# Optimization experiments

Hardware: AMD Instinct MI355X
Metric: run time of the kernel (lower is better)

Reference implementation:

```python
import jax, jax.numpy as jnp
import numpy as np

B, T, C = 4, 2048, 1024


def wkv(k, v, w, u, reverse):
    """RWKV WKV scan with running-max stabilization.
    k, v: [B, T, C]; w, u: [C]. Returns y: [B, T, C]."""
    def step(carry, kv):
        num, den, mx = carry          # each [B, C]
        k_t, v_t = kv                 # each [B, C]
        ku = k_t + u
        m = jnp.maximum(mx, ku)
        e1 = jnp.exp(mx - m)
        e2 = jnp.exp(ku - m)
        y = (e1 * num + e2 * v_t) / (e1 * den + e2)
        # state update with decay w
        mw = mx + w
        mn = jnp.maximum(mw, k_t)
        e1s = jnp.exp(mw - mn)
        e2s = jnp.exp(k_t - mn)
        return (e1s * num + e2s * v_t, e1s * den + e2s, mn), y

    z = jnp.zeros_like(k[:, 0])
    init = (z, z, jnp.full_like(z, -1e38))
    ks = jnp.swapaxes(k, 0, 1)  # [T, B, C]
    vs = jnp.swapaxes(v, 0, 1)
    _, ys = jax.lax.scan(step, init, (ks, vs), reverse=reverse)
    return jnp.swapaxes(ys, 0, 1)


def setup_inputs() -> dict:
    key = jax.random.key(0)
    k1, k2, k3, k4, k5, k6, k7 = jax.random.split(key, 7)
    x = jax.random.normal(k1, (B, T, C), dtype=jnp.float32)
    rkv_w = jax.random.normal(k2, (6 * C, C), dtype=jnp.float32) / np.sqrt(C)
    out_w = jax.random.normal(k3, (C, 2 * C), dtype=jnp.float32) / np.sqrt(2 * C)
    time_decay = jax.random.uniform(k4, (C,), jnp.float32, -6.0, -5.0)
    time_first = jax.random.uniform(k5, (C,), jnp.float32, -3.0, 0.0)
    time_decay_rev = jax.random.uniform(k6, (C,), jnp.float32, -6.0, -5.0)
    time_first_rev = jax.random.uniform(k7, (C,), jnp.float32, -3.0, 0.0)
    return {"x": x, "rkv_w": rkv_w, "out_w": out_w,
            "time_decay": time_decay, "time_first": time_first,
            "time_decay_rev": time_decay_rev, "time_first_rev": time_first_rev}


def reference(x, rkv_w, out_w, time_decay, time_first, time_decay_rev, time_first_rev):
    b, t, c = x.shape
    rkv = jnp.einsum('btc,dc->btd', x, rkv_w).reshape(b, t, 2, 3, c)
    r_f, k_f, v_f = rkv[:, :, 0, 0], rkv[:, :, 0, 1], rkv[:, :, 0, 2]
    r_b, k_b, v_b = rkv[:, :, 1, 0], rkv[:, :, 1, 1], rkv[:, :, 1, 2]
    out_f = jax.nn.sigmoid(r_f) * wkv(k_f, v_f, -jnp.exp(time_decay), time_first, False)
    out_b = jax.nn.sigmoid(r_b) * wkv(k_b, v_b, -jnp.exp(time_decay_rev), time_first_rev, True)
    out_cat = jnp.concatenate([out_f, out_b], axis=-1)  # [B, T, 2C]
    return jnp.einsum('btd,cd->btc', out_cat, out_w)
```

## Files before the change

### kernel.cpp

```cpp
#include <hip/hip_runtime.h>
#include <cstdint>
#include <cstddef>

#define Bdim 4
#define Tdim 2048
#define Cdim 1024

#define SEG  16
#define CHB  32
#define LSEG (Tdim / SEG)

typedef __attribute__((ext_vector_type(8))) short bf16x8;
typedef __attribute__((ext_vector_type(4))) float f32x4;

__device__ __forceinline__ unsigned short f2bf(float f) {
    unsigned int u = __float_as_uint(f);
    u += 0x7fffu + ((u >> 16) & 1u);
    return (unsigned short)(u >> 16);
}
__device__ __forceinline__ float bf2f(unsigned short h) {
    return __uint_as_float((unsigned int)h << 16);
}

__device__ __forceinline__ void gload_lds16(const void* g, void* l) {
    __builtin_amdgcn_global_load_lds(
        (const __attribute__((address_space(1))) unsigned int*)g,
        (__attribute__((address_space(3))) unsigned int*)l,
        16, 0, 0);
}

__global__ __launch_bounds__(256) void cast_f32_bf16(
    const float* __restrict__ in, unsigned short* __restrict__ out, int n4)
{
    int i = blockIdx.x * 256 + threadIdx.x;
    if (i >= n4) return;
    float4 v = ((const float4*)in)[i];
    ushort4 o;
    o.x = f2bf(v.x); o.y = f2bf(v.y); o.z = f2bf(v.z); o.w = f2bf(v.w);
    ((ushort4*)out)[i] = o;
}

__device__ __forceinline__ void stage_half(
    const unsigned short* __restrict__ G, int row0, int K, int elemoff,
    char* slot, int wave, int lane)
{
    const int sl = (lane & 3) ^ ((lane >> 3) & 3);
    const unsigned short* gp = G + (size_t)(row0 + wave * 16 + (lane >> 2)) * K
                                 + elemoff + sl * 8;
    gload_lds16(gp, slot + wave * 1024);
    gload_lds16(gp + (size_t)128 * K, slot + 8192 + wave * 1024);
}

#define GPHASE(D, KH, MH, SG, SROW0, SOFF, SSLOT, VM)                          \
  {                                                                            \
    const char* As_ = ldsb + (D)*32768 + (KH)*16384;                           \
    const char* Bs_ = ldsb + 65536 + (D)*32768 + (KH)*16384;                   \
    bf16x8 a_[4], b_[4];                                                       \
    _Pragma("unroll")                                                          \
    for (int i_ = 0; i_ < 4; ++i_)                                             \
      a_[i_] = *(const bf16x8*)(As_ + (wm*128 + ((MH)*4+i_)*16 + fr)*64 + cswz);\
    _Pragma("unroll")                                                          \
    for (int j_ = 0; j_ < 4; ++j_)                                             \
      b_[j_] = *(const bf16x8*)(Bs_ + (wn*64 + j_*16 + fr)*64 + cswz);         \
    stage_half(SG, SROW0, K, SOFF, SSLOT, wave, lane);                         \
    __builtin_amdgcn_s_barrier();                                              \
    __builtin_amdgcn_sched_barrier(0);                                         \
    __builtin_amdgcn_s_setprio(1);                                             \
    _Pragma("unroll")                                                          \
    for (int i_ = 0; i_ < 4; ++i_)                                             \
      _Pragma("unroll")                                                        \
      for (int j_ = 0; j_ < 4; ++j_)                                           \
        acc[(MH)*4+i_][j_] = __builtin_amdgcn_mfma_f32_16x16x32_bf16(          \
            a_[i_], b_[j_], acc[(MH)*4+i_][j_], 0, 0, 0);                      \
    __builtin_amdgcn_s_setprio(0);                                             \
    if (VM) { asm volatile("s_waitcnt vmcnt(8)" ::: "memory"); }               \
    __builtin_amdgcn_s_barrier();                                              \
    __builtin_amdgcn_sched_barrier(0);                                         \
  }

__global__ __launch_bounds__(512, 2) void gemm_bf16_nt_256_obf(
    const unsigned short* __restrict__ A, const unsigned short* __restrict__ B,
    unsigned short* __restrict__ C, int M, int N, int K, int gx)
{
    __shared__ char ldsbuf[131072];
    char* ldsb = ldsbuf;

    const int tid  = threadIdx.x;
    const int wave = tid >> 6;
    const int lane = tid & 63;
    const int wm = wave >> 2;
    const int wn = wave & 3;
    const int fr = lane & 15;
    const int cswz = (((lane >> 4) ^ ((fr >> 1) & 3)) << 4);

    const int nwg = gridDim.x;
    const int cpx = nwg >> 3;
    const int b0  = blockIdx.x;
    const int swz = (b0 & 7) * cpx + (b0 >> 3);
    const int bx  = swz % gx;
    const int by  = swz / gx;
    const int m0 = by * 256;
    const int n0 = bx * 256;

    const int NKT = K >> 6;
    const int NI  = K >> 7;

    f32x4 acc[8][4] = {};

    stage_half(A, m0, K, 0,  ldsb + 0,             wave, lane);
    stage_half(B, n0, K, 0,  ldsb + 65536,         wave, lane);
    stage_half(A, m0, K, 32, ldsb + 16384,         wave, lane);
    stage_half(B, n0, K, 32, ldsb + 65536 + 16384, wave, lane);
    stage_half(A, m0, K, 64, ldsb + 32768,         wave, lane);
    stage_half(B, n0, K, 64, ldsb + 65536 + 32768, wave, lane);
    asm volatile("s_waitcnt vmcnt(8)" ::: "memory");
    __builtin_amdgcn_s_barrier();
    __builtin_amdgcn_sched_barrier(0);

    for (int i = 0; i < NI; ++i) {
        const int k1e = (2 * i + 1) * 64;
        int k2 = 2 * i + 2; if (k2 >= NKT) k2 = NKT - 1;
        int k3 = 2 * i + 3; if (k3 >= NKT) k3 = NKT - 1;
        const int k2e = k2 * 64, k3e = k3 * 64;

        GPHASE(0, 0, 0, A, m0, k1e + 32, ldsb + 32768 + 16384,         0)
        GPHASE(0, 0, 1, B, n0, k1e + 32, ldsb + 65536 + 32768 + 16384, 1)
        GPHASE(0, 1, 0, A, m0, k2e,      ldsb + 0,                     0)
        GPHASE(0, 1, 1, B, n0, k2e,      ldsb + 65536,                 1)
        GPHASE(1, 0, 0, A, m0, k2e + 32, ldsb + 16384,                 0)
        GPHASE(1, 0, 1, B, n0, k2e + 32, ldsb + 65536 + 16384,         1)
        GPHASE(1, 1, 0, A, m0, k3e,      ldsb + 32768,                 0)
        GPHASE(1, 1, 1, B, n0, k3e,      ldsb + 65536 + 32768,         1)
    }

    #pragma unroll
    for (int mi = 0; mi < 8; ++mi) {
        const int row = m0 + wm * 128 + mi * 16 + (lane >> 4) * 4;
        #pragma unroll
        for (int nj = 0; nj < 4; ++nj) {
            const int col = n0 + wn * 64 + nj * 16 + fr;
            #pragma unroll
            for (int r = 0; r < 4; ++r)
                C[(size_t)(row + r) * N + col] = f2bf(acc[mi][nj][r]);
        }
    }
}

__global__ __launch_bounds__(256) void gemm_bf16_nt(
    const unsigned short* __restrict__ A, const unsigned short* __restrict__ B,
    float* __restrict__ C, int M, int N, int K)
{
    __shared__ unsigned short As[128 * 32];
    __shared__ unsigned short Bs[128 * 32];

    const int tid  = threadIdx.x;
    const int wave = tid >> 6;
    const int lane = tid & 63;
    const int m0 = blockIdx.y * 128;
    const int n0 = blockIdx.x * 128;
    const int wr = wave >> 1, wc = wave & 1;

    const int srow = tid >> 2;
    const int scol = (tid & 3) * 8;
    const unsigned short* Ag = A + (size_t)(m0 + srow) * K + scol;
    const unsigned short* Bg = B + (size_t)(n0 + srow) * K + scol;
    char* AsW = (char*)As + wave * 1024;
    char* BsW = (char*)Bs + wave * 1024;

    f32x4 acc[4][4] = {};

    const int fr = lane & 15;
    const int fk = (lane >> 4) * 8;

    for (int k0 = 0; k0 < K; k0 += 32) {
        gload_lds16(Ag + k0,                  AsW);
        gload_lds16(Ag + k0 + (size_t)64 * K, AsW + 4096);
        gload_lds16(Bg + k0,                  BsW);
        gload_lds16(Bg + k0 + (size_t)64 * K, BsW + 4096);
        __syncthreads();

        bf16x8 af[4], bfr_[4];
        #pragma unroll
        for (int f = 0; f < 4; ++f) {
            af[f]   = *(const bf16x8*)&As[(wr * 64 + f * 16 + fr) * 32 + fk];
            bfr_[f] = *(const bf16x8*)&Bs[(wc * 64 + f * 16 + fr) * 32 + fk];
        }
        #pragma unroll
        for (int i = 0; i < 4; ++i)
            #pragma unroll
            for (int j = 0; j < 4; ++j)
                acc[i][j] = __builtin_amdgcn_mfma_f32_16x16x32_bf16(
                    af[i], bfr_[j], acc[i][j], 0, 0, 0);
        __syncthreads();
    }

    #pragma unroll
    for (int i = 0; i < 4; ++i) {
        const int row = m0 + wr * 64 + i * 16 + (lane >> 4) * 4;
        #pragma unroll
        for (int j = 0; j < 4; ++j) {
            const int col = n0 + wc * 64 + j * 16 + (lane & 15);
            #pragma unroll
            for (int r = 0; r < 4; ++r)
                C[(size_t)(row + r) * N + col] = acc[i][j][r];
        }
    }
}

__global__ __launch_bounds__(512) void wkv_scan_par(
    const unsigned short* __restrict__ rkv,
    const float* __restrict__ td,  const float* __restrict__ tf,
    const float* __restrict__ tdr, const float* __restrict__ tfr,
    unsigned short* __restrict__ outcat)
{
    __shared__ float sBn[SEG][CHB], sBd[SEG][CHB], sMb[SEG][CHB];

    const int tid = threadIdx.x;
    const int ch  = tid & (CHB - 1);
    const int seg = tid >> 5;

    const int bi  = blockIdx.x;
    const int b   = bi >> 6;
    const int rem = bi & 63;
    const int dir = rem >> 5;
    const int c   = (rem & 31) * CHB + ch;

    const float w = -__expf(dir ? tdr[c] : td[c]);
    const float u = dir ? tfr[c] : tf[c];

    const int strideT = 6 * Cdim;
    const int tstep   = dir ? -strideT : strideT;
    const int t0      = dir ? (Tdim - 1 - seg * LSEG) : (seg * LSEG);

    const unsigned short* pbase = rkv + ((size_t)b * Tdim + t0) * strideT + dir * 3 * Cdim + c;

    const int PF = 4;

    float bn = 0.0f, bd = 0.0f, mb = -1e38f;
    {
        const unsigned short* q = pbase;
        float kk[PF], vv[PF];
        #pragma unroll
        for (int i = 0; i < PF; ++i) {
            kk[i] = bf2f(q[Cdim]); vv[i] = bf2f(q[2 * Cdim]); q += tstep;
        }
        for (int t = 0; t < LSEG; t += PF) {
            float kn[PF], vn[PF];
            if (t + PF < LSEG) {
                #pragma unroll
                for (int i = 0; i < PF; ++i) {
                    kn[i] = bf2f(q[Cdim]); vn[i] = bf2f(q[2 * Cdim]); q += tstep;
                }
            }
            #pragma unroll
            for (int i = 0; i < PF; ++i) {
                const float k_ = kk[i], v_ = vv[i];
                const float mw = mb + w;
                const float mn = fmaxf(mw, k_);
                const float e1 = __expf(mw - mn);
                const float e2 = __expf(k_ - mn);
                bn = e1 * bn + e2 * v_;
                bd = e1 * bd + e2;
                mb = mn;
            }
            #pragma unroll
            for (int i = 0; i < PF; ++i) { kk[i] = kn[i]; vv[i] = vn[i]; }
        }
    }
    sBn[seg][ch] = bn; sBd[seg][ch] = bd; sMb[seg][ch] = mb;
    __syncthreads();

    if (tid < CHB) {
        float n = 0.0f, d = 0.0f, m = -1e38f;
        const float a = w * (float)LSEG;
        for (int s = 0; s < SEG; ++s) {
            const float tn = sBn[s][tid], tdn = sBd[s][tid], tm = sMb[s][tid];
            sBn[s][tid] = n; sBd[s][tid] = d; sMb[s][tid] = m;
            const float ma = m + a;
            const float mm = fmaxf(ma, tm);
            const float e1 = __expf(ma - mm);
            const float e2 = __expf(tm - mm);
            n = e1 * n + e2 * tn;
            d = e1 * d + e2 * tdn;
            m = mm;
        }
    }
    __syncthreads();

    float num = sBn[seg][ch], den = sBd[seg][ch], mx = sMb[seg][ch];
    {
        const unsigned short* q = pbase;
        unsigned short* po = outcat + ((size_t)b * Tdim + t0) * (2 * Cdim) + dir * Cdim + c;
        const int ostep = dir ? -(2 * Cdim) : (2 * Cdim);

        float rr[PF], kk[PF], vv[PF];
        #pragma unroll
        for (int i = 0; i < PF; ++i) {
            rr[i] = bf2f(q[0]); kk[i] = bf2f(q[Cdim]); vv[i] = bf2f(q[2 * Cdim]); q += tstep;
        }
        for (int t = 0; t < LSEG; t += PF) {
            float rn[PF], kn[PF], vn[PF];
            if (t + PF < LSEG) {
                #pragma unroll
                for (int i = 0; i < PF; ++i) {
                    rn[i] = bf2f(q[0]); kn[i] = bf2f(q[Cdim]); vn[i] = bf2f(q[2 * Cdim]); q += tstep;
                }
            }
            #pragma unroll
            for (int i = 0; i < PF; ++i) {
                const float k_ = kk[i], v_ = vv[i], r_ = rr[i];
                const float ku = k_ + u;
                const float m  = fmaxf(mx, ku);
                const float e1 = __expf(mx - m);
                const float e2 = __expf(ku - m);
                const float y  = (e1 * num + e2 * v_) / (e1 * den + e2);
                const float sr = 1.0f / (1.0f + __expf(-r_));
                *po = f2bf(sr * y);
                po += ostep;
                const float mw  = mx + w;
                const float mn  = fmaxf(mw, k_);
                const float e1s = __expf(mw - mn);
                const float e2s = __expf(k_ - mn);
                num = e1s * num + e2s * v_;
                den = e1s * den + e2s;
                mx  = mn;
            }
            #pragma unroll
            for (int i = 0; i < PF; ++i) { rr[i] = rn[i]; kk[i] = kn[i]; vv[i] = vn[i]; }
        }
    }
}

extern "C" void kernel_launch(void* const* d_in, const int* in_sizes, int n_in,
                              void* d_out, int out_size, void* d_ws, size_t ws_size,
                              hipStream_t stream)
{
    const float* x    = (const float*)d_in[0];
    const float* rkvw = (const float*)d_in[1];
    const float* outw = (const float*)d_in[2];
    const float* td   = (const float*)d_in[3];
    const float* tf   = (const float*)d_in[4];
    const float* tdr  = (const float*)d_in[5];
    const float* tfr  = (const float*)d_in[6];
    float* out = (float*)d_out;

    const int M = Bdim * Tdim;

    char* ws = (char*)d_ws;
    unsigned short* rkv = (unsigned short*)ws;
    unsigned short* xb  = (unsigned short*)(ws + 100663296);
    unsigned short* wb  = (unsigned short*)(ws + 117440512);
    unsigned short* ob  = (unsigned short*)(ws + 130023424);
    unsigned short* cat = (unsigned short*)(ws + 134217728);

    dim3 blk(256);

    hipLaunchKernelGGL(cast_f32_bf16, dim3((M * Cdim / 4 + 255) / 256), blk, 0, stream,
                       x, xb, M * Cdim / 4);
    hipLaunchKernelGGL(cast_f32_bf16, dim3((6 * Cdim * Cdim / 4 + 255) / 256), blk, 0, stream,
                       rkvw, wb, 6 * Cdim * Cdim / 4);
    hipLaunchKernelGGL(cast_f32_bf16, dim3((Cdim * 2 * Cdim / 4 + 255) / 256), blk, 0, stream,
                       outw, ob, Cdim * 2 * Cdim / 4);

    hipLaunchKernelGGL(gemm_bf16_nt_256_obf, dim3((6 * Cdim / 256) * (M / 256)), dim3(512),
                       0, stream, xb, wb, rkv, M, 6 * Cdim, Cdim, 6 * Cdim / 256);

    hipLaunchKernelGGL(wkv_scan_par, dim3(Bdim * 2 * (Cdim / CHB)), dim3(512), 0, stream,
                       rkv, td, tf, tdr, tfr, cat);

    hipLaunchKernelGGL(gemm_bf16_nt, dim3(Cdim / 128, M / 128), blk, 0, stream,
                       cat, ob, out, M, Cdim, 2 * Cdim);
}
```

Measured before the change: 259.2 us.

## Make projection GEMM persistent over three tiles and double WKV scan segments

The input projection GEMM becomes a persistent kernel with 256 workgroups, each handling three 256x256 output tiles. Its LDS prefetch pipeline runs straight across tile boundaries, so the next tile's loads overlap the current tile's epilogue and the pipeline is filled once instead of per tile. The WKV scan now uses 32 time segments per block (1024 threads) and a deeper prefetch of 8 steps, giving more parallelism in the chunked scan. The cost is occupancy: launch bounds drop to one 512-thread block per CU for the GEMM, and the scan's larger blocks raise register pressure.

```diff
diff --git a/kernel.cpp b/kernel.cpp
--- a/kernel.cpp
+++ b/kernel.cpp
@@ -6,9 +6,16 @@
 #define Tdim 2048
 #define Cdim 1024
 
-#define SEG  16
+#define SEG  32
 #define CHB  32
 #define LSEG (Tdim / SEG)
+
+#define G1_K    1024
+#define G1_GX   24
+#define G1_CPX  96
+#define G1_NIPT 8
+#define G1_NITER 24
+#define G1_GMAX 47
 
 typedef __attribute__((ext_vector_type(8))) short bf16x8;
 typedef __attribute__((ext_vector_type(4))) float f32x4;
@@ -51,7 +58,7 @@
     gload_lds16(gp + (size_t)128 * K, slot + 8192 + wave * 1024);
 }
 
-#define GPHASE(D, KH, MH, SG, SROW0, SOFF, SSLOT, VM)                          \
+#define GP(D, KH, MH, GPTR, ROW0, ELEMOFF, SSLOT, VM)                          \
   {                                                                            \
     const char* As_ = ldsb + (D)*32768 + (KH)*16384;                           \
     const char* Bs_ = ldsb + 65536 + (D)*32768 + (KH)*16384;                   \
@@ -62,7 +69,7 @@
     _Pragma("unroll")                                                          \
     for (int j_ = 0; j_ < 4; ++j_)                                             \
       b_[j_] = *(const bf16x8*)(Bs_ + (wn*64 + j_*16 + fr)*64 + cswz);         \
-    stage_half(SG, SROW0, K, SOFF, SSLOT, wave, lane);                         \
+    stage_half(GPTR, ROW0, G1_K, ELEMOFF, SSLOT, wave, lane);                  \
     __builtin_amdgcn_s_barrier();                                              \
     __builtin_amdgcn_sched_barrier(0);                                         \
     __builtin_amdgcn_s_setprio(1);                                             \
@@ -78,9 +85,11 @@
     __builtin_amdgcn_sched_barrier(0);                                         \
   }
 
-__global__ __launch_bounds__(512, 2) void gemm_bf16_nt_256_obf(
+#define SELJ(j, a0, a1, a2) ((j) == 0 ? (a0) : ((j) == 1 ? (a1) : (a2)))
+
+__global__ __launch_bounds__(512, 1) void gemm1_persist(
     const unsigned short* __restrict__ A, const unsigned short* __restrict__ B,
-    unsigned short* __restrict__ C, int M, int N, int K, int gx)
+    unsigned short* __restrict__ C, int N)
 {
     __shared__ char ldsbuf[131072];
     char* ldsb = ldsbuf;
@@ -93,55 +102,72 @@
     const int fr = lane & 15;
     const int cswz = (((lane >> 4) ^ ((fr >> 1) & 3)) << 4);
 
-    const int nwg = gridDim.x;
-    const int cpx = nwg >> 3;
-    const int b0  = blockIdx.x;
-    const int swz = (b0 & 7) * cpx + (b0 >> 3);
-    const int bx  = swz % gx;
-    const int by  = swz / gx;
-    const int m0 = by * 256;
-    const int n0 = bx * 256;
-
-    const int NKT = K >> 6;
-    const int NI  = K >> 7;
+    int m0j[1], n0j[1];
+    int m0_0, n0_0, m0_1, n0_1, m0_2, n0_2;
+    {
+        int vb, swz;
+        vb = blockIdx.x;          swz = (vb & 7) * G1_CPX + (vb >> 3);
+        m0_0 = (swz / G1_GX) * 256; n0_0 = (swz % G1_GX) * 256;
+        vb = blockIdx.x + 256;    swz = (vb & 7) * G1_CPX + (vb >> 3);
+        m0_1 = (swz / G1_GX) * 256; n0_1 = (swz % G1_GX) * 256;
+        vb = blockIdx.x + 512;    swz = (vb & 7) * G1_CPX + (vb >> 3);
+        m0_2 = (swz / G1_GX) * 256; n0_2 = (swz % G1_GX) * 256;
+    }
+    (void)m0j; (void)n0j;
 
     f32x4 acc[8][4] = {};
 
-    stage_half(A, m0, K, 0,  ldsb + 0,             wave, lane);
-    stage_half(B, n0, K, 0,  ldsb + 65536,         wave, lane);
-    stage_half(A, m0, K, 32, ldsb + 16384,         wave, lane);
-    stage_half(B, n0, K, 32, ldsb + 65536 + 16384, wave, lane);
-    stage_half(A, m0, K, 64, ldsb + 32768,         wave, lane);
-    stage_half(B, n0, K, 64, ldsb + 65536 + 32768, wave, lane);
+    stage_half(A, m0_0, G1_K, 0,  ldsb + 0,             wave, lane);
+    stage_half(B, n0_0, G1_K, 0,  ldsb + 65536,         wave, lane);
+    stage_half(A, m0_0, G1_K, 32, ldsb + 16384,         wave, lane);
+    stage_half(B, n0_0, G1_K, 32, ldsb + 65536 + 16384, wave, lane);
+    stage_half(A, m0_0, G1_K, 64, ldsb + 32768,         wave, lane);
+    stage_half(B, n0_0, G1_K, 64, ldsb + 65536 + 32768, wave, lane);
     asm volatile("s_waitcnt vmcnt(8)" ::: "memory");
     __builtin_amdgcn_s_barrier();
     __builtin_amdgcn_sched_barrier(0);
 
-    for (int i = 0; i < NI; ++i) {
-        const int k1e = (2 * i + 1) * 64;
-        int k2 = 2 * i + 2; if (k2 >= NKT) k2 = NKT - 1;
-        int k3 = 2 * i + 3; if (k3 >= NKT) k3 = NKT - 1;
-        const int k2e = k2 * 64, k3e = k3 * 64;
-
-        GPHASE(0, 0, 0, A, m0, k1e + 32, ldsb + 32768 + 16384,         0)
-        GPHASE(0, 0, 1, B, n0, k1e + 32, ldsb + 65536 + 32768 + 16384, 1)
-        GPHASE(0, 1, 0, A, m0, k2e,      ldsb + 0,                     0)
-        GPHASE(0, 1, 1, B, n0, k2e,      ldsb + 65536,                 1)
-        GPHASE(1, 0, 0, A, m0, k2e + 32, ldsb + 16384,                 0)
-        GPHASE(1, 0, 1, B, n0, k2e + 32, ldsb + 65536 + 16384,         1)
-        GPHASE(1, 1, 0, A, m0, k3e,      ldsb + 32768,                 0)
-        GPHASE(1, 1, 1, B, n0, k3e,      ldsb + 65536 + 32768,         1)
-    }
-
-    #pragma unroll
-    for (int mi = 0; mi < 8; ++mi) {
-        const int row = m0 + wm * 128 + mi * 16 + (lane >> 4) * 4;
-        #pragma unroll
-        for (int nj = 0; nj < 4; ++nj) {
-            const int col = n0 + wn * 64 + nj * 16 + fr;
-            #pragma unroll
-            for (int r = 0; r < 4; ++r)
-                C[(size_t)(row + r) * N + col] = f2bf(acc[mi][nj][r]);
+    for (int i = 0; i < G1_NITER; ++i) {
+        const int jc  = i >> 3;
+        int g2 = 2 * i + 2; if (g2 > G1_GMAX) g2 = G1_GMAX;
+        int g3 = 2 * i + 3; if (g3 > G1_GMAX) g3 = G1_GMAX;
+        const int j2 = g2 >> 4, kt2 = g2 & 15;
+        const int j3 = g3 >> 4, kt3 = g3 & 15;
+        const int kt1 = (2 * i + 1) & 15;
+
+        const int m0c = SELJ(jc, m0_0, m0_1, m0_2);
+        const int n0c = SELJ(jc, n0_0, n0_1, n0_2);
+        const int m02 = SELJ(j2, m0_0, m0_1, m0_2);
+        const int n02 = SELJ(j2, n0_0, n0_1, n0_2);
+        const int m03 = SELJ(j3, m0_0, m0_1, m0_2);
+        const int n03 = SELJ(j3, n0_0, n0_1, n0_2);
+
+        GP(0, 0, 0, A, m0c, kt1 * 64 + 32, ldsb + 32768 + 16384,         0)
+        GP(0, 0, 1, B, n0c, kt1 * 64 + 32, ldsb + 65536 + 32768 + 16384, 1)
+        GP(0, 1, 0, A, m02, kt2 * 64,      ldsb + 0,                     0)
+        GP(0, 1, 1, B, n02, kt2 * 64,      ldsb + 65536,                 1)
+        GP(1, 0, 0, A, m02, kt2 * 64 + 32, ldsb + 16384,                 0)
+        GP(1, 0, 1, B, n02, kt2 * 64 + 32, ldsb + 65536 + 16384,         1)
+        GP(1, 1, 0, A, m03, kt3 * 64,      ldsb + 32768,                 0)
+        GP(1, 1, 1, B, n03, kt3 * 64,      ldsb + 65536 + 32768,         1)
+
+        if ((i & 7) == 7) {
+            #pragma unroll
+            for (int mi = 0; mi < 8; ++mi) {
+                const int row = m0c + wm * 128 + mi * 16 + (lane >> 4) * 4;
+                #pragma unroll
+                for (int nj = 0; nj < 4; ++nj) {
+                    const int col = n0c + wn * 64 + nj * 16 + fr;
+                    #pragma unroll
+                    for (int r = 0; r < 4; ++r)
+                        C[(size_t)(row + r) * N + col] = f2bf(acc[mi][nj][r]);
+                }
+            }
+            #pragma unroll
+            for (int mi = 0; mi < 8; ++mi)
+                #pragma unroll
+                for (int nj = 0; nj < 4; ++nj)
+                    acc[mi][nj] = (f32x4){0.f, 0.f, 0.f, 0.f};
         }
     }
 }
@@ -207,7 +233,7 @@
     }
 }
 
-__global__ __launch_bounds__(512) void wkv_scan_par(
+__global__ __launch_bounds__(1024) void wkv_scan_par(
     const unsigned short* __restrict__ rkv,
     const float* __restrict__ td,  const float* __restrict__ tf,
     const float* __restrict__ tdr, const float* __restrict__ tfr,
@@ -234,7 +260,7 @@
 
     const unsigned short* pbase = rkv + ((size_t)b * Tdim + t0) * strideT + dir * 3 * Cdim + c;
 
-    const int PF = 4;
+    const int PF = 8;
 
     float bn = 0.0f, bd = 0.0f, mb = -1e38f;
     {
@@ -362,10 +388,10 @@
     hipLaunchKernelGGL(cast_f32_bf16, dim3((Cdim * 2 * Cdim / 4 + 255) / 256), blk, 0, stream,
                        outw, ob, Cdim * 2 * Cdim / 4);
 
-    hipLaunchKernelGGL(gemm_bf16_nt_256_obf, dim3((6 * Cdim / 256) * (M / 256)), dim3(512),
-                       0, stream, xb, wb, rkv, M, 6 * Cdim, Cdim, 6 * Cdim / 256);
-
-    hipLaunchKernelGGL(wkv_scan_par, dim3(Bdim * 2 * (Cdim / CHB)), dim3(512), 0, stream,
+    hipLaunchKernelGGL(gemm1_persist, dim3(256), dim3(512), 0, stream,
+                       xb, wb, rkv, 6 * Cdim);
+
+    hipLaunchKernelGGL(wkv_scan_par, dim3(Bdim * 2 * (Cdim / CHB)), dim3(1024), 0, stream,
                        rkv, td, tf, tdr, tfr, cat);
 
     hipLaunchKernelGGL(gemm_bf16_nt, dim3(Cdim / 128, M / 128), blk, 0, stream,
```

Measured after the change: 253.5 us. 2.2% less time.
